# Performance work log

Hardware: AMD Instinct MI355X
Metric: run time of the kernel (lower is better)

## Reference

```python
import jax, jax.numpy as jnp
import numpy as np

# Model dims / constants (from par in init_kwargs)
B, N_IN, NN = 128, 1024, 512
DT, TAU_M, V_TH = 0.05, 10.0, 2.0
ALPHA = 1.0 - DT / TAU_M  # leak factor, 0.995


def setup_inputs() -> dict:
    key = jax.random.key(0)
    k1, k2, k3, k4 = jax.random.split(key, 4)
    x = jax.random.normal(k1, (B, N_IN, NN), dtype=jnp.float32)          # input traces per neuron
    w = jax.random.normal(k2, (N_IN, NN), dtype=jnp.float32) / np.sqrt(N_IN)  # init.normal_(std=1/sqrt(n_in))
    v = jax.random.normal(k3, (B, NN), dtype=jnp.float32)                # membrane potential state
    z = (jax.random.uniform(k4, (B, NN)) < 0.1).astype(jnp.float32)      # previous spikes (0/1)
    return {"x": x, "w": w, "v": v, "z": z}


def reference(x, w, v, z):
    # LIF membrane update, vectorized over the batch (original uses a per-batch Python loop):
    #   v[b] = alpha*v[b] + sum_i x[b,i,:]*w[i,:] - v_th*z[b].detach()
    v_new = ALPHA * v + jnp.sum(x * w[None, :, :], axis=1) - V_TH * jax.lax.stop_gradient(z)
    # threshold nonlinearity -> output spikes
    z_new = (v_new - V_TH > 0).astype(v_new.dtype)
    return v_new, z_new
```

## Files before the change

kernel.cpp:

```cpp
#include <hip/hip_runtime.h>


constexpr int B    = 128;
constexpr int N_IN = 1024;
constexpr int NN   = 512;
constexpr int NN4  = NN / 4;
constexpr float ALPHA = 1.0f - 0.05f / 10.0f;
constexpr float V_TH  = 2.0f;

__global__ __launch_bounds__(256) void lif_fused(
    const float4* __restrict__ x4,
    const float4* __restrict__ w4,
    const float4* __restrict__ v4,
    const float4* __restrict__ z4,
    float4* __restrict__ vout4,
    float4* __restrict__ zout4)
{
    const int t    = threadIdx.x;
    const int g    = t & 15;
    const int c    = t >> 4;
    const int b    = blockIdx.x >> 3;
    const int slab = blockIdx.x & 7;
    const int n4   = slab * 16 + g;

    const float4* __restrict__ xp =
        x4 + (size_t)b * N_IN * NN4 + (size_t)(c * 64) * NN4 + n4;
    const float4* __restrict__ wp =
        w4 + (size_t)(c * 64) * NN4 + n4;

    float ax = 0.f, ay = 0.f, az = 0.f, aw = 0.f;
    #pragma unroll 8
    for (int ii = 0; ii < 64; ++ii) {
        float4 xv = xp[(size_t)ii * NN4];
        float4 wv = wp[(size_t)ii * NN4];
        ax = fmaf(xv.x, wv.x, ax);
        ay = fmaf(xv.y, wv.y, ay);
        az = fmaf(xv.z, wv.z, az);
        aw = fmaf(xv.w, wv.w, aw);
    }

    __shared__ float4 red[256];
    red[t] = make_float4(ax, ay, az, aw);
    __syncthreads();

    #pragma unroll
    for (int s = 128; s >= 16; s >>= 1) {
        if (t < s) {
            float4 a = red[t], o = red[t + s];
            a.x += o.x; a.y += o.y; a.z += o.z; a.w += o.w;
            red[t] = a;
        }
        __syncthreads();
    }

    if (t < 16) {
        float4 a = red[t];
        const int col = slab * 16 + t;
        const int idx = b * NN4 + col;
        float4 vv = v4[idx];
        float4 zz = z4[idx];
        float4 vn;
        vn.x = fmaf(ALPHA, vv.x, a.x) - V_TH * zz.x;
        vn.y = fmaf(ALPHA, vv.y, a.y) - V_TH * zz.y;
        vn.z = fmaf(ALPHA, vv.z, a.z) - V_TH * zz.z;
        vn.w = fmaf(ALPHA, vv.w, a.w) - V_TH * zz.w;
        vout4[idx] = vn;
        float4 zn;
        zn.x = (vn.x - V_TH > 0.f) ? 1.f : 0.f;
        zn.y = (vn.y - V_TH > 0.f) ? 1.f : 0.f;
        zn.z = (vn.z - V_TH > 0.f) ? 1.f : 0.f;
        zn.w = (vn.w - V_TH > 0.f) ? 1.f : 0.f;
        zout4[idx] = zn;
    }
}

extern "C" void kernel_launch(void* const* d_in, const int* in_sizes, int n_in,
                              void* d_out, int out_size, void* d_ws, size_t ws_size,
                              hipStream_t stream) {
    const float4* x = (const float4*)d_in[0];
    const float4* w = (const float4*)d_in[1];
    const float4* v = (const float4*)d_in[2];
    const float4* z = (const float4*)d_in[3];
    float4* vout = (float4*)d_out;
    float4* zout = vout + (size_t)B * NN4;

    lif_fused<<<dim3(B * 8), dim3(256), 0, stream>>>(x, w, v, z, vout, zout);
}
```

Baseline: 49.15 us.

## Split reduction into partial-sum and finalize kernels with batch-pair weight reuse

Measured after the change: 48.84 us. About the same (-0.6%).

```diff
diff --git a/kernel.cpp b/kernel.cpp
--- a/kernel.cpp
+++ b/kernel.cpp
@@ -1,5 +1,7 @@
 #include <hip/hip_runtime.h>
 
+
+typedef float f32x4 __attribute__((ext_vector_type(4)));
 
 constexpr int B    = 128;
 constexpr int N_IN = 1024;
@@ -8,81 +10,96 @@
 constexpr float ALPHA = 1.0f - 0.05f / 10.0f;
 constexpr float V_TH  = 2.0f;
 
-__global__ __launch_bounds__(256) void lif_fused(
-    const float4* __restrict__ x4,
-    const float4* __restrict__ w4,
-    const float4* __restrict__ v4,
-    const float4* __restrict__ z4,
-    float4* __restrict__ vout4,
-    float4* __restrict__ zout4)
+__global__ __launch_bounds__(256) void lif_partial(
+    const f32x4* __restrict__ x4,
+    const f32x4* __restrict__ w4,
+    f32x4* __restrict__ part)
 {
     const int t    = threadIdx.x;
-    const int g    = t & 15;
-    const int c    = t >> 4;
-    const int b    = blockIdx.x >> 3;
-    const int slab = blockIdx.x & 7;
-    const int n4   = slab * 16 + g;
+    const int g    = t & 63;
+    const int c    = t >> 6;
+    const int sub  = blockIdx.x & 15;
+    const int bp   = blockIdx.x >> 4;
+    const int slab = sub & 1;
+    const int ig   = sub >> 1;
 
-    const float4* __restrict__ xp =
-        x4 + (size_t)b * N_IN * NN4 + (size_t)(c * 64) * NN4 + n4;
-    const float4* __restrict__ wp =
-        w4 + (size_t)(c * 64) * NN4 + n4;
+    const int b0  = bp * 2;
+    const int col = slab * 64 + g;
+    const int i0  = ig * 128 + c * 32;
 
-    float ax = 0.f, ay = 0.f, az = 0.f, aw = 0.f;
+    const f32x4* __restrict__ xp0 =
+        x4 + ((size_t)b0 * N_IN + i0) * NN4 + col;
+    const f32x4* __restrict__ xp1 = xp0 + (size_t)N_IN * NN4;
+    const f32x4* __restrict__ wp  = w4 + (size_t)i0 * NN4 + col;
+
+    f32x4 a0 = {0.f, 0.f, 0.f, 0.f};
+    f32x4 a1 = {0.f, 0.f, 0.f, 0.f};
     #pragma unroll 8
-    for (int ii = 0; ii < 64; ++ii) {
-        float4 xv = xp[(size_t)ii * NN4];
-        float4 wv = wp[(size_t)ii * NN4];
-        ax = fmaf(xv.x, wv.x, ax);
-        ay = fmaf(xv.y, wv.y, ay);
-        az = fmaf(xv.z, wv.z, az);
-        aw = fmaf(xv.w, wv.w, aw);
+    for (int ii = 0; ii < 32; ++ii) {
+        f32x4 wv  = wp[(size_t)ii * NN4];
+        f32x4 xv0 = __builtin_nontemporal_load(&xp0[(size_t)ii * NN4]);
+        f32x4 xv1 = __builtin_nontemporal_load(&xp1[(size_t)ii * NN4]);
+        a0 += xv0 * wv;
+        a1 += xv1 * wv;
     }
 
-    __shared__ float4 red[256];
-    red[t] = make_float4(ax, ay, az, aw);
+    __shared__ f32x4 red0[256];
+    __shared__ f32x4 red1[256];
+    red0[t] = a0;
+    red1[t] = a1;
     __syncthreads();
 
+    if (t < 128) {
+        red0[t] += red0[t + 128];
+        red1[t] += red1[t + 128];
+    }
+    __syncthreads();
+    if (t < 64) {
+        f32x4 s0 = red0[t] + red0[t + 64];
+        f32x4 s1 = red1[t] + red1[t + 64];
+        const int cidx = slab * 64 + t;
+        part[((size_t)ig * B + b0)     * NN4 + cidx] = s0;
+        part[((size_t)ig * B + b0 + 1) * NN4 + cidx] = s1;
+    }
+}
+
+__global__ __launch_bounds__(256) void lif_finalize(
+    const f32x4* __restrict__ part,
+    const f32x4* __restrict__ v4,
+    const f32x4* __restrict__ z4,
+    f32x4* __restrict__ vout4,
+    f32x4* __restrict__ zout4)
+{
+    const int idx = blockIdx.x * 256 + threadIdx.x;
+    if (idx >= B * NN4) return;
+    f32x4 s = part[idx];
     #pragma unroll
-    for (int s = 128; s >= 16; s >>= 1) {
-        if (t < s) {
-            float4 a = red[t], o = red[t + s];
-            a.x += o.x; a.y += o.y; a.z += o.z; a.w += o.w;
-            red[t] = a;
-        }
-        __syncthreads();
-    }
-
-    if (t < 16) {
-        float4 a = red[t];
-        const int col = slab * 16 + t;
-        const int idx = b * NN4 + col;
-        float4 vv = v4[idx];
-        float4 zz = z4[idx];
-        float4 vn;
-        vn.x = fmaf(ALPHA, vv.x, a.x) - V_TH * zz.x;
-        vn.y = fmaf(ALPHA, vv.y, a.y) - V_TH * zz.y;
-        vn.z = fmaf(ALPHA, vv.z, a.z) - V_TH * zz.z;
-        vn.w = fmaf(ALPHA, vv.w, a.w) - V_TH * zz.w;
-        vout4[idx] = vn;
-        float4 zn;
-        zn.x = (vn.x - V_TH > 0.f) ? 1.f : 0.f;
-        zn.y = (vn.y - V_TH > 0.f) ? 1.f : 0.f;
-        zn.z = (vn.z - V_TH > 0.f) ? 1.f : 0.f;
-        zn.w = (vn.w - V_TH > 0.f) ? 1.f : 0.f;
-        zout4[idx] = zn;
-    }
+    for (int igr = 1; igr < 8; ++igr)
+        s += part[(size_t)igr * B * NN4 + idx];
+    f32x4 vv = v4[idx];
+    f32x4 zz = z4[idx];
+    f32x4 vn = ALPHA * vv + s - V_TH * zz;
+    vout4[idx] = vn;
+    f32x4 zn;
+    zn.x = (vn.x - V_TH > 0.f) ? 1.f : 0.f;
+    zn.y = (vn.y - V_TH > 0.f) ? 1.f : 0.f;
+    zn.z = (vn.z - V_TH > 0.f) ? 1.f : 0.f;
+    zn.w = (vn.w - V_TH > 0.f) ? 1.f : 0.f;
+    zout4[idx] = zn;
 }
 
 extern "C" void kernel_launch(void* const* d_in, const int* in_sizes, int n_in,
                               void* d_out, int out_size, void* d_ws, size_t ws_size,
                               hipStream_t stream) {
-    const float4* x = (const float4*)d_in[0];
-    const float4* w = (const float4*)d_in[1];
-    const float4* v = (const float4*)d_in[2];
-    const float4* z = (const float4*)d_in[3];
-    float4* vout = (float4*)d_out;
-    float4* zout = vout + (size_t)B * NN4;
+    const f32x4* x = (const f32x4*)d_in[0];
+    const f32x4* w = (const f32x4*)d_in[1];
+    const f32x4* v = (const f32x4*)d_in[2];
+    const f32x4* z = (const f32x4*)d_in[3];
+    f32x4* vout = (f32x4*)d_out;
+    f32x4* zout = vout + (size_t)B * NN4;
+    f32x4* part = (f32x4*)d_ws;
 
-    lif_fused<<<dim3(B * 8), dim3(256), 0, stream>>>(x, w, v, z, vout, zout);
+    lif_partial<<<dim3(64 * 16), dim3(256), 0, stream>>>(x, w, part);
+    lif_finalize<<<dim3((B * NN4 + 255) / 256), dim3(256), 0, stream>>>(
+        part, v, z, vout, zout);
 }
```
